# Optimization experiments

Measured on AMD Instinct MI355X. Metric: run time of the kernel, lower is better.

Reference implementation:

```python
import jax, jax.numpy as jnp
import numpy as np
import math

WINDOW = 7
NUM_HEADS = 8


def setup_inputs() -> dict:
    key = jax.random.key(0)
    k0, k1, k2 = jax.random.split(key, 3)
    E = 256
    x = jax.random.normal(k0, (64, 3136, E), dtype=jnp.float32)
    in_proj_w = jax.random.normal(k1, (3 * E, E), dtype=jnp.float32) * 0.02
    in_proj_b = jnp.zeros((3 * E,), dtype=jnp.float32)
    out_w = jax.random.normal(k2, (E, E), dtype=jnp.float32) * 0.02
    out_b = jnp.zeros((E,), dtype=jnp.float32)
    return {"x": x, "in_proj_w": in_proj_w, "in_proj_b": in_proj_b,
            "out_w": out_w, "out_b": out_b}


def _window_partition(x, k):
    # Faithful to torch: transpose->reshape to image, F.unfold(kernel=stride=k),
    # then reshape(bs*nw, k*k, C). Note unfold row order is (c, ky, kx), so the
    # final reshape intentionally reproduces torch's channel-major scramble.
    bs, N, C = x.shape
    H = int(math.sqrt(N))
    nw = (H // k) * (H // k)
    img = jnp.transpose(x, (0, 2, 1)).reshape(bs, C, H, H)
    # (bs, C, Hk, k, Wk, k) -> (bs, Hk, Wk, C, k, k)
    win = img.reshape(bs, C, H // k, k, H // k, k).transpose(0, 2, 4, 1, 3, 5)
    # contiguous flatten of (C,k,k) == unfold row order; reshape to (k*k, C)
    return win.reshape(bs * nw, k * k, C), bs, nw


def _mha(win, in_proj_w, in_proj_b, out_w, out_b, h):
    M, L, E = win.shape
    d = E // h
    qkv = win @ in_proj_w.T + in_proj_b          # (M, L, 3E)
    q, k, v = jnp.split(qkv, 3, axis=-1)
    q = q.reshape(M, L, h, d)
    k = k.reshape(M, L, h, d)
    v = v.reshape(M, L, h, d)
    scores = jnp.einsum('mqhd,mkhd->mhqk', q, k) / jnp.sqrt(jnp.float32(d))
    attn = jax.nn.softmax(scores, axis=-1)       # (M, h, L, L)
    o = jnp.einsum('mhqk,mkhd->mqhd', attn, v).reshape(M, L, E)
    o = o @ out_w.T + out_b
    return o, attn.mean(axis=1)                  # avg over heads (torch default)


def reference(x, in_proj_w, in_proj_b, out_w, out_b):
    win, bs, nw = _window_partition(x, WINDOW)
    o, attn_w = _mha(win, in_proj_w, in_proj_b, out_w, out_b, NUM_HEADS)
    L = WINDOW * WINDOW
    y = o.reshape(bs, nw, L, x.shape[-1])
    return y, attn_w
```

## Files before the change

### kernel.cpp

```cpp
#include <hip/hip_runtime.h>
#include <hip/hip_bf16.h>


typedef float  f32x4  __attribute__((ext_vector_type(4)));
typedef short  s16x8  __attribute__((ext_vector_type(8)));
typedef short  s16x4  __attribute__((ext_vector_type(4)));

#define MFMA16(a, b, c) __builtin_amdgcn_mfma_f32_16x16x32_bf16((a), (b), (c), 0, 0, 0)

static __device__ __forceinline__ unsigned short f2bf(float f) {
    __hip_bfloat16 h = __float2bfloat16(f);
    unsigned short u;
    __builtin_memcpy(&u, &h, 2);
    return u;
}

#define SMEM_BYTES 61440

__global__ __launch_bounds__(256, 2)
void wmha_fused_kernel(const float* __restrict__ x,
                       const float* __restrict__ bqkv,
                       const float* __restrict__ bout,
                       const unsigned short* __restrict__ wq,
                       const unsigned short* __restrict__ wo,
                       float* __restrict__ yout,
                       float* __restrict__ aout)
{
    extern __shared__ char smem[];
    unsigned short* winb = (unsigned short*)smem;
    unsigned short* Qb   = (unsigned short*)(smem + 33792);
    unsigned short* Kb   = (unsigned short*)(smem + 43008);
    unsigned short* VTb  = (unsigned short*)(smem + 52224);
    float* stg = (float*)(smem + 33792);

    const int tid  = threadIdx.x;
    const int wave = tid >> 6;
    const int lane = tid & 63;
    const int lx   = lane & 15;
    const int lg   = lane >> 4;
    const int h    = wave & 1;
    const int mh   = wave >> 1;

    const int m  = blockIdx.x;
    const int b  = m >> 6;
    const int w  = m & 63;
    const int hk = w >> 3;
    const int wk = w & 7;
    const float* xb = x + (size_t)b * 3136 * 256;

    for (int p = wave; p < 49; p += 4) {
        const int ky = p / 7, kx = p - ky * 7;
        const int rimg = (hk * 7 + ky) * 56 + wk * 7 + kx;
        const float4 v = *(const float4*)&xb[rimg * 256 + lane * 4];
        #pragma unroll
        for (int e = 0; e < 4; ++e) {
            const int j = (lane * 4 + e) * 49 + p;
            winb[(j >> 8) * 264 + (j & 255)] = f2bf(e == 0 ? v.x : e == 1 ? v.y : e == 2 ? v.z : v.w);
        }
    }
    for (int i = tid; i < 15 * 256; i += 256)
        winb[(49 + (i >> 8)) * 264 + (i & 255)] = 0;
    __syncthreads();

    s16x8 afrag[4][8];
    #pragma unroll
    for (int mt = 0; mt < 4; ++mt)
        #pragma unroll
        for (int ks = 0; ks < 8; ++ks)
            afrag[mt][ks] = *(const s16x8*)&winb[(lx + mt * 16) * 264 + ks * 32 + lg * 8];
    __syncthreads();

    unsigned short* ob = winb;
    unsigned short* Ph = (h == 0) ? Qb : Kb;
    const float scale = 0.17677669529663687f;
    float pacc[2][4][4] = {};

    for (int hp = 0; hp < 4; ++hp) {
        #pragma unroll
        for (int i = 0; i < 3; ++i) {
            const int t = wave * 3 + i;
            const int part = t >> 2;
            const int sub  = t & 3;
            const int n0 = part * 256 + hp * 64 + sub * 16;
            f32x4 acc[4] = {};
            const unsigned short* wp = wq + (size_t)(n0 + lx) * 256 + lg * 8;
            #pragma unroll
            for (int ks = 0; ks < 8; ++ks) {
                const s16x8 bb = *(const s16x8*)(wp + ks * 32);
                #pragma unroll
                for (int mt = 0; mt < 4; ++mt)
                    acc[mt] = MFMA16(afrag[mt][ks], bb, acc[mt]);
            }
            const float bias = bqkv[n0 + lx];
            if (part == 0) {
                #pragma unroll
                for (int mt = 0; mt < 4; ++mt)
                    #pragma unroll
                    for (int r = 0; r < 4; ++r)
                        Qb[(mt * 16 + lg * 4 + r) * 72 + sub * 16 + lx] =
                            f2bf((acc[mt][r] + bias) * scale);
            } else if (part == 1) {
                #pragma unroll
                for (int mt = 0; mt < 4; ++mt)
                    #pragma unroll
                    for (int r = 0; r < 4; ++r)
                        Kb[(mt * 16 + lg * 4 + r) * 72 + sub * 16 + lx] =
                            f2bf(acc[mt][r] + bias);
            } else {
                #pragma unroll
                for (int mt = 0; mt < 4; ++mt) {
                    s16x4 pk;
                    #pragma unroll
                    for (int r = 0; r < 4; ++r)
                        pk[r] = (short)f2bf(acc[mt][r] + bias);
                    *(s16x4*)&VTb[(sub * 16 + lx) * 72 + mt * 16 + lg * 4] = pk;
                }
            }
        }
        __syncthreads();

        s16x8 qa[2];
        #pragma unroll
        for (int mt = 0; mt < 2; ++mt)
            qa[mt] = *(const s16x8*)&Qb[(mh * 32 + mt * 16 + lx) * 72 + h * 32 + lg * 8];
        f32x4 sacc[2][4] = {};
        #pragma unroll
        for (int nt = 0; nt < 4; ++nt) {
            const s16x8 kb = *(const s16x8*)&Kb[(nt * 16 + lx) * 72 + h * 32 + lg * 8];
            #pragma unroll
            for (int mt = 0; mt < 2; ++mt)
                sacc[mt][nt] = MFMA16(qa[mt], kb, sacc[mt][nt]);
        }

        float pv[2][4][4];
        #pragma unroll
        for (int mt = 0; mt < 2; ++mt) {
            #pragma unroll
            for (int r = 0; r < 4; ++r) {
                const bool ok3 = (lx == 0);
                float e0 = __expf(sacc[mt][0][r]);
                float e1 = __expf(sacc[mt][1][r]);
                float e2 = __expf(sacc[mt][2][r]);
                float e3 = ok3 ? __expf(sacc[mt][3][r]) : 0.f;
                float sum = e0 + e1 + e2 + e3;
                #pragma unroll
                for (int s = 1; s < 16; s <<= 1) sum += __shfl_xor(sum, s);
                const float inv = 1.0f / sum;
                pv[mt][r][0] = e0 * inv;
                pv[mt][r][1] = e1 * inv;
                pv[mt][r][2] = e2 * inv;
                pv[mt][r][3] = e3 * inv;
                #pragma unroll
                for (int nt = 0; nt < 4; ++nt)
                    pacc[mt][r][nt] += pv[mt][r][nt] * 0.125f;
            }
        }
        __syncthreads();

        #pragma unroll
        for (int mt = 0; mt < 2; ++mt)
            #pragma unroll
            for (int r = 0; r < 4; ++r) {
                const int q = mh * 32 + mt * 16 + lg * 4 + r;
                #pragma unroll
                for (int nt = 0; nt < 4; ++nt)
                    Ph[q * 72 + nt * 16 + lx] = f2bf(pv[mt][r][nt]);
            }
        s16x8 pa[2][2], vb[2][2];
        #pragma unroll
        for (int mt = 0; mt < 2; ++mt)
            #pragma unroll
            for (int ks = 0; ks < 2; ++ks)
                pa[mt][ks] = *(const s16x8*)&Ph[(mh * 32 + mt * 16 + lx) * 72 + ks * 32 + lg * 8];
        #pragma unroll
        for (int nt = 0; nt < 2; ++nt)
            #pragma unroll
            for (int ks = 0; ks < 2; ++ks)
                vb[nt][ks] = *(const s16x8*)&VTb[(h * 32 + nt * 16 + lx) * 72 + ks * 32 + lg * 8];
        f32x4 oacc[2][2] = {};
        #pragma unroll
        for (int ks = 0; ks < 2; ++ks)
            #pragma unroll
            for (int mt = 0; mt < 2; ++mt)
                #pragma unroll
                for (int nt = 0; nt < 2; ++nt)
                    oacc[mt][nt] = MFMA16(pa[mt][ks], vb[nt][ks], oacc[mt][nt]);
        #pragma unroll
        for (int mt = 0; mt < 2; ++mt)
            #pragma unroll
            for (int nt = 0; nt < 2; ++nt)
                #pragma unroll
                for (int r = 0; r < 4; ++r)
                    ob[(mh * 32 + mt * 16 + lg * 4 + r) * 264 +
                       hp * 64 + h * 32 + nt * 16 + lx] = f2bf(oacc[mt][nt][r]);
        __syncthreads();
    }

    if (h == 0) {
        #pragma unroll
        for (int mt = 0; mt < 2; ++mt)
            #pragma unroll
            for (int r = 0; r < 4; ++r) {
                const int row = mh * 32 + mt * 16 + lg * 4 + r;
                #pragma unroll
                for (int nt = 0; nt < 4; ++nt)
                    stg[row * 66 + nt * 16 + lx] = pacc[mt][r][nt];
            }
    }
    #pragma unroll
    for (int mt = 0; mt < 4; ++mt)
        #pragma unroll
        for (int ks = 0; ks < 8; ++ks)
            afrag[mt][ks] = *(const s16x8*)&ob[(lx + mt * 16) * 264 + ks * 32 + lg * 8];
    __syncthreads();

    if (h == 1) {
        float* abase = aout + (size_t)m * 2401;
        #pragma unroll
        for (int mt = 0; mt < 2; ++mt)
            #pragma unroll
            for (int r = 0; r < 4; ++r) {
                const int q = mh * 32 + mt * 16 + lg * 4 + r;
                if (q < 49) {
                    #pragma unroll
                    for (int nt = 0; nt < 4; ++nt) {
                        const int col = nt * 16 + lx;
                        if (col < 49)
                            abase[q * 49 + col] = stg[q * 66 + col] + pacc[mt][r][nt];
                    }
                }
            }
    }

    float* ybase = yout + (size_t)m * 12544;
    #pragma unroll
    for (int nt = 0; nt < 4; ++nt) {
        const int n0 = wave * 64 + nt * 16;
        f32x4 acc[4] = {};
        const unsigned short* wp = wo + (size_t)(n0 + lx) * 256 + lg * 8;
        #pragma unroll
        for (int ks = 0; ks < 8; ++ks) {
            const s16x8 bb = *(const s16x8*)(wp + ks * 32);
            #pragma unroll
            for (int mt = 0; mt < 4; ++mt)
                acc[mt] = MFMA16(afrag[mt][ks], bb, acc[mt]);
        }
        const float bias = bout[n0 + lx];
        #pragma unroll
        for (int mt = 0; mt < 4; ++mt) {
            #pragma unroll
            for (int r = 0; r < 4; ++r) {
                const int q = mt * 16 + lg * 4 + r;
                if (q < 49) ybase[q * 256 + n0 + lx] = acc[mt][r] + bias;
            }
        }
    }
}

__global__ void wmha_cvt_kernel(const float* __restrict__ w_in,
                                const float* __restrict__ w_out,
                                unsigned short* __restrict__ dq,
                                unsigned short* __restrict__ dw)
{
    const int idx = blockIdx.x * 256 + threadIdx.x;
    if (idx < 196608)      dq[idx] = f2bf(w_in[idx]);
    else                   dw[idx - 196608] = f2bf(w_out[idx - 196608]);
}

extern "C" void kernel_launch(void* const* d_in, const int* in_sizes, int n_in,
                              void* d_out, int out_size, void* d_ws, size_t ws_size,
                              hipStream_t stream) {
    const float* x    = (const float*)d_in[0];
    const float* w_in = (const float*)d_in[1];
    const float* b_in = (const float*)d_in[2];
    const float* w_o  = (const float*)d_in[3];
    const float* b_o  = (const float*)d_in[4];

    unsigned short* wq_bf = (unsigned short*)d_ws;
    unsigned short* wo_bf = wq_bf + 196608;

    float* y  = (float*)d_out;
    float* aw = y + (size_t)4096 * 49 * 256;

    wmha_cvt_kernel<<<1024, 256, 0, stream>>>(w_in, w_o, wq_bf, wo_bf);

    hipFuncSetAttribute((const void*)wmha_fused_kernel,
                        hipFuncAttributeMaxDynamicSharedMemorySize, SMEM_BYTES);
    wmha_fused_kernel<<<4096, 256, SMEM_BYTES, stream>>>(
        x, b_in, b_o, wq_bf, wo_bf, y, aw);
}
```

Before: 423.0 us.

## Interleave QKV/out-proj MFMA chains, per-wave P buffers, padded LDS strides

Reworks the fused windowed-MHA kernel in several ways. The QKV and output projections now issue three or four independent accumulator chains per k-step, which raises instruction-level parallelism and lets weight loads overlap. The softmax output P goes to a private per-wave LDS buffer, removing one block-wide barrier per head pair. LDS strides change (264→260, 72→76) to shift bank mapping, and the window gather now uses all threads with vectorised zero padding. The extra LDS (about 80KB per block) and larger accumulator register footprint may reduce occupancy under launch_bounds(256,2).

```diff
diff --git a/kernel.cpp b/kernel.cpp
--- a/kernel.cpp
+++ b/kernel.cpp
@@ -15,7 +15,9 @@
     return u;
 }
 
-#define SMEM_BYTES 61440
+#define SMEM_BYTES 80896
+#define WS 260
+#define QS 76
 
 __global__ __launch_bounds__(256, 2)
 void wmha_fused_kernel(const float* __restrict__ x,
@@ -28,10 +30,10 @@
 {
     extern __shared__ char smem[];
     unsigned short* winb = (unsigned short*)smem;
-    unsigned short* Qb   = (unsigned short*)(smem + 33792);
+    unsigned short* Qb   = (unsigned short*)(smem + 33280);
     unsigned short* Kb   = (unsigned short*)(smem + 43008);
-    unsigned short* VTb  = (unsigned short*)(smem + 52224);
-    float* stg = (float*)(smem + 33792);
+    unsigned short* VTb  = (unsigned short*)(smem + 52736);
+    float* stg = (float*)(smem + 33280);
 
     const int tid  = threadIdx.x;
     const int wave = tid >> 6;
@@ -41,6 +43,8 @@
     const int h    = wave & 1;
     const int mh   = wave >> 1;
 
+    unsigned short* Pw = (unsigned short*)(smem + 62464 + wave * 4608);
+
     const int m  = blockIdx.x;
     const int b  = m >> 6;
     const int w  = m & 63;
@@ -48,18 +52,32 @@
     const int wk = w & 7;
     const float* xb = x + (size_t)b * 3136 * 256;
 
-    for (int p = wave; p < 49; p += 4) {
-        const int ky = p / 7, kx = p - ky * 7;
-        const int rimg = (hk * 7 + ky) * 56 + wk * 7 + kx;
-        const float4 v = *(const float4*)&xb[rimg * 256 + lane * 4];
-        #pragma unroll
-        for (int e = 0; e < 4; ++e) {
-            const int j = (lane * 4 + e) * 49 + p;
-            winb[(j >> 8) * 264 + (j & 255)] = f2bf(e == 0 ? v.x : e == 1 ? v.y : e == 2 ? v.z : v.w);
-        }
-    }
-    for (int i = tid; i < 15 * 256; i += 256)
-        winb[(49 + (i >> 8)) * 264 + (i & 255)] = 0;
+    #pragma unroll
+    for (int ii = 0; ii < 13; ++ii) {
+        const int k = tid + ii * 256;
+        if (k < 3136) {
+            const int p  = k >> 6;
+            const int l4 = (k & 63) * 4;
+            const int ky = p / 7, kx = p - ky * 7;
+            const int rimg = (hk * 7 + ky) * 56 + wk * 7 + kx;
+            const float4 v = *(const float4*)&xb[rimg * 256 + l4];
+            #pragma unroll
+            for (int e = 0; e < 4; ++e) {
+                const int j = (l4 + e) * 49 + p;
+                winb[(j >> 8) * WS + (j & 255)] =
+                    f2bf(e == 0 ? v.x : e == 1 ? v.y : e == 2 ? v.z : v.w);
+            }
+        }
+    }
+    #pragma unroll
+    for (int ii = 0; ii < 4; ++ii) {
+        const int i = tid + ii * 256;
+        if (i < 960) {
+            const int row = 49 + (i >> 6);
+            const int c4  = (i & 63) * 4;
+            *(s16x4*)&winb[row * WS + c4] = (s16x4){0, 0, 0, 0};
+        }
+    }
     __syncthreads();
 
     s16x8 afrag[4][8];
@@ -67,53 +85,64 @@
     for (int mt = 0; mt < 4; ++mt)
         #pragma unroll
         for (int ks = 0; ks < 8; ++ks)
-            afrag[mt][ks] = *(const s16x8*)&winb[(lx + mt * 16) * 264 + ks * 32 + lg * 8];
+            afrag[mt][ks] = *(const s16x8*)&winb[(lx + mt * 16) * WS + ks * 32 + lg * 8];
     __syncthreads();
 
     unsigned short* ob = winb;
-    unsigned short* Ph = (h == 0) ? Qb : Kb;
     const float scale = 0.17677669529663687f;
     float pacc[2][4][4] = {};
 
+    #pragma unroll 1
     for (int hp = 0; hp < 4; ++hp) {
-        #pragma unroll
-        for (int i = 0; i < 3; ++i) {
-            const int t = wave * 3 + i;
-            const int part = t >> 2;
-            const int sub  = t & 3;
-            const int n0 = part * 256 + hp * 64 + sub * 16;
-            f32x4 acc[4] = {};
-            const unsigned short* wp = wq + (size_t)(n0 + lx) * 256 + lg * 8;
-            #pragma unroll
-            for (int ks = 0; ks < 8; ++ks) {
-                const s16x8 bb = *(const s16x8*)(wp + ks * 32);
-                #pragma unroll
-                for (int mt = 0; mt < 4; ++mt)
-                    acc[mt] = MFMA16(afrag[mt][ks], bb, acc[mt]);
-            }
-            const float bias = bqkv[n0 + lx];
+        const int t0 = wave * 3;
+        const unsigned short* wp[3];
+        float bias[3];
+        #pragma unroll
+        for (int j = 0; j < 3; ++j) {
+            const int t = t0 + j;
+            const int n0 = (t >> 2) * 256 + hp * 64 + (t & 3) * 16;
+            wp[j]   = wq + (size_t)(n0 + lx) * 256 + lg * 8;
+            bias[j] = bqkv[n0 + lx];
+        }
+        f32x4 acc[3][4] = {};
+        #pragma unroll
+        for (int ks = 0; ks < 8; ++ks) {
+            const s16x8 bb0 = *(const s16x8*)(wp[0] + ks * 32);
+            const s16x8 bb1 = *(const s16x8*)(wp[1] + ks * 32);
+            const s16x8 bb2 = *(const s16x8*)(wp[2] + ks * 32);
+            #pragma unroll
+            for (int mt = 0; mt < 4; ++mt) {
+                acc[0][mt] = MFMA16(afrag[mt][ks], bb0, acc[0][mt]);
+                acc[1][mt] = MFMA16(afrag[mt][ks], bb1, acc[1][mt]);
+                acc[2][mt] = MFMA16(afrag[mt][ks], bb2, acc[2][mt]);
+            }
+        }
+        #pragma unroll
+        for (int j = 0; j < 3; ++j) {
+            const int t = t0 + j;
+            const int part = t >> 2, sub = t & 3;
             if (part == 0) {
                 #pragma unroll
                 for (int mt = 0; mt < 4; ++mt)
                     #pragma unroll
                     for (int r = 0; r < 4; ++r)
-                        Qb[(mt * 16 + lg * 4 + r) * 72 + sub * 16 + lx] =
-                            f2bf((acc[mt][r] + bias) * scale);
+                        Qb[(mt * 16 + lg * 4 + r) * QS + sub * 16 + lx] =
+                            f2bf((acc[j][mt][r] + bias[j]) * scale);
             } else if (part == 1) {
                 #pragma unroll
                 for (int mt = 0; mt < 4; ++mt)
                     #pragma unroll
                     for (int r = 0; r < 4; ++r)
-                        Kb[(mt * 16 + lg * 4 + r) * 72 + sub * 16 + lx] =
-                            f2bf(acc[mt][r] + bias);
+                        Kb[(mt * 16 + lg * 4 + r) * QS + sub * 16 + lx] =
+                            f2bf(acc[j][mt][r] + bias[j]);
             } else {
                 #pragma unroll
                 for (int mt = 0; mt < 4; ++mt) {
                     s16x4 pk;
                     #pragma unroll
                     for (int r = 0; r < 4; ++r)
-                        pk[r] = (short)f2bf(acc[mt][r] + bias);
-                    *(s16x4*)&VTb[(sub * 16 + lx) * 72 + mt * 16 + lg * 4] = pk;
+                        pk[r] = (short)f2bf(acc[j][mt][r] + bias[j]);
+                    *(s16x4*)&VTb[(sub * 16 + lx) * QS + mt * 16 + lg * 4] = pk;
                 }
             }
         }
@@ -122,11 +151,11 @@
         s16x8 qa[2];
         #pragma unroll
         for (int mt = 0; mt < 2; ++mt)
-            qa[mt] = *(const s16x8*)&Qb[(mh * 32 + mt * 16 + lx) * 72 + h * 32 + lg * 8];
+            qa[mt] = *(const s16x8*)&Qb[(mh * 32 + mt * 16 + lx) * QS + h * 32 + lg * 8];
         f32x4 sacc[2][4] = {};
         #pragma unroll
         for (int nt = 0; nt < 4; ++nt) {
-            const s16x8 kb = *(const s16x8*)&Kb[(nt * 16 + lx) * 72 + h * 32 + lg * 8];
+            const s16x8 kb = *(const s16x8*)&Kb[(nt * 16 + lx) * QS + h * 32 + lg * 8];
             #pragma unroll
             for (int mt = 0; mt < 2; ++mt)
                 sacc[mt][nt] = MFMA16(qa[mt], kb, sacc[mt][nt]);
@@ -155,28 +184,28 @@
                     pacc[mt][r][nt] += pv[mt][r][nt] * 0.125f;
             }
         }
-        __syncthreads();
-
-        #pragma unroll
-        for (int mt = 0; mt < 2; ++mt)
-            #pragma unroll
-            for (int r = 0; r < 4; ++r) {
-                const int q = mh * 32 + mt * 16 + lg * 4 + r;
+
+        #pragma unroll
+        for (int mt = 0; mt < 2; ++mt)
+            #pragma unroll
+            for (int r = 0; r < 4; ++r) {
+                const int qr = mt * 16 + lg * 4 + r;
                 #pragma unroll
                 for (int nt = 0; nt < 4; ++nt)
-                    Ph[q * 72 + nt * 16 + lx] = f2bf(pv[mt][r][nt]);
-            }
+                    Pw[qr * 72 + nt * 16 + lx] = f2bf(pv[mt][r][nt]);
+            }
+
         s16x8 pa[2][2], vb[2][2];
         #pragma unroll
         for (int mt = 0; mt < 2; ++mt)
             #pragma unroll
             for (int ks = 0; ks < 2; ++ks)
-                pa[mt][ks] = *(const s16x8*)&Ph[(mh * 32 + mt * 16 + lx) * 72 + ks * 32 + lg * 8];
+                pa[mt][ks] = *(const s16x8*)&Pw[(mt * 16 + lx) * 72 + ks * 32 + lg * 8];
         #pragma unroll
         for (int nt = 0; nt < 2; ++nt)
             #pragma unroll
             for (int ks = 0; ks < 2; ++ks)
-                vb[nt][ks] = *(const s16x8*)&VTb[(h * 32 + nt * 16 + lx) * 72 + ks * 32 + lg * 8];
+                vb[nt][ks] = *(const s16x8*)&VTb[(h * 32 + nt * 16 + lx) * QS + ks * 32 + lg * 8];
         f32x4 oacc[2][2] = {};
         #pragma unroll
         for (int ks = 0; ks < 2; ++ks)
@@ -191,7 +220,7 @@
             for (int nt = 0; nt < 2; ++nt)
                 #pragma unroll
                 for (int r = 0; r < 4; ++r)
-                    ob[(mh * 32 + mt * 16 + lg * 4 + r) * 264 +
+                    ob[(mh * 32 + mt * 16 + lg * 4 + r) * WS +
                        hp * 64 + h * 32 + nt * 16 + lx] = f2bf(oacc[mt][nt][r]);
         __syncthreads();
     }
@@ -211,7 +240,7 @@
     for (int mt = 0; mt < 4; ++mt)
         #pragma unroll
         for (int ks = 0; ks < 8; ++ks)
-            afrag[mt][ks] = *(const s16x8*)&ob[(lx + mt * 16) * 264 + ks * 32 + lg * 8];
+            afrag[mt][ks] = *(const s16x8*)&ob[(lx + mt * 16) * WS + ks * 32 + lg * 8];
     __syncthreads();
 
     if (h == 1) {
@@ -233,25 +262,32 @@
     }
 
     float* ybase = yout + (size_t)m * 12544;
+    const int n0w = wave * 64;
+    const unsigned short* wp2 = wo + (size_t)(n0w + lx) * 256 + lg * 8;
+    f32x4 acc2[4][4] = {};
+    #pragma unroll
+    for (int ks = 0; ks < 8; ++ks) {
+        const s16x8 b0 = *(const s16x8*)(wp2 +     0 + ks * 32);
+        const s16x8 b1 = *(const s16x8*)(wp2 +  4096 + ks * 32);
+        const s16x8 b2 = *(const s16x8*)(wp2 +  8192 + ks * 32);
+        const s16x8 b3 = *(const s16x8*)(wp2 + 12288 + ks * 32);
+        #pragma unroll
+        for (int mt = 0; mt < 4; ++mt) {
+            acc2[0][mt] = MFMA16(afrag[mt][ks], b0, acc2[0][mt]);
+            acc2[1][mt] = MFMA16(afrag[mt][ks], b1, acc2[1][mt]);
+            acc2[2][mt] = MFMA16(afrag[mt][ks], b2, acc2[2][mt]);
+            acc2[3][mt] = MFMA16(afrag[mt][ks], b3, acc2[3][mt]);
+        }
+    }
     #pragma unroll
     for (int nt = 0; nt < 4; ++nt) {
-        const int n0 = wave * 64 + nt * 16;
-        f32x4 acc[4] = {};
-        const unsigned short* wp = wo + (size_t)(n0 + lx) * 256 + lg * 8;
-        #pragma unroll
-        for (int ks = 0; ks < 8; ++ks) {
-            const s16x8 bb = *(const s16x8*)(wp + ks * 32);
-            #pragma unroll
-            for (int mt = 0; mt < 4; ++mt)
-                acc[mt] = MFMA16(afrag[mt][ks], bb, acc[mt]);
-        }
-        const float bias = bout[n0 + lx];
+        const float bias = bout[n0w + nt * 16 + lx];
         #pragma unroll
         for (int mt = 0; mt < 4; ++mt) {
             #pragma unroll
             for (int r = 0; r < 4; ++r) {
                 const int q = mt * 16 + lg * 4 + r;
-                if (q < 49) ybase[q * 256 + n0 + lx] = acc[mt][r] + bias;
+                if (q < 49) ybase[q * 256 + n0w + nt * 16 + lx] = acc2[nt][mt][r] + bias;
             }
         }
     }
```

Result: slower. 563.1 us (+33.1%).
